# Performance work log

Measured on AMD Instinct MI355X. Metric: run time of the kernel, lower is better.

The kernel has to match this reference:

```python
import jax, jax.numpy as jnp
import numpy as np
from jax.scipy.special import logsumexp

K, V, D, R = 512, 50257, 768, 192
S_ITERS = 10
LAMBDA_MAHAL = 0.3
GAMMA_SINKHORN = 0.3


def setup_inputs() -> dict:
    key = jax.random.key(0)
    ks = jax.random.split(key, 6)
    word_embeds = jax.random.normal(ks[0], (V, D), dtype=jnp.float32)
    # warm-start anchors: mean word embed + small noise (as in torch init)
    anchors = jnp.broadcast_to(word_embeds.mean(axis=0, keepdims=True), (K, D)) \
        + jax.random.normal(ks[1], (K, D), dtype=jnp.float32) * 0.05
    return {
        "word_embeds": word_embeds,
        "concept_anchors": anchors,
        "M_U": jax.random.normal(ks[2], (D, R), dtype=jnp.float32) * 0.01,
        "log_eps": jnp.float32(-1.5),
        "log_scale": jnp.float32(0.0),
        "topic_bias": jnp.zeros((K, 1), dtype=jnp.float32),
        "word_proj_w": jnp.eye(D, dtype=jnp.float32),
    }


def _normalize(x, eps=1e-12):
    n = jnp.sqrt(jnp.sum(x * x, axis=-1, keepdims=True))
    return x / jnp.maximum(n, eps)


def _mahalanobis_cost(A, B, M_U):
    # M = I + U U^T  (low-rank update); C[k,v] = (a-b)^T M (a-b)
    M = jnp.eye(A.shape[-1], dtype=A.dtype) + M_U @ M_U.T
    MA = A @ M          # [K, D]
    MB = B @ M          # [V, D]
    AA = jnp.sum(MA * A, axis=-1, keepdims=True)       # [K, 1]
    BB = jnp.sum(MB * B, axis=-1, keepdims=True).T     # [1, V]
    AB = MA @ B.T                                      # [K, V]
    return jax.nn.relu(AA + BB - 2.0 * AB)


def _sinkhorn_log(log_K):
    def body(_, carry):
        log_u, log_v = carry
        log_u = -logsumexp(log_K + log_v, axis=1, keepdims=True)  # [K,1]
        log_v = -logsumexp(log_K + log_u, axis=0, keepdims=True)  # [1,V]
        return log_u, log_v
    log_u0 = jnp.zeros((log_K.shape[0], 1), log_K.dtype)
    log_v0 = jnp.zeros((1, log_K.shape[1]), log_K.dtype)
    log_u, log_v = jax.lax.fori_loop(0, S_ITERS, body, (log_u0, log_v0))
    return log_K + log_u + log_v


def reference(word_embeds, concept_anchors, M_U, log_eps, log_scale,
              topic_bias, word_proj_w):
    w = _normalize(word_embeds @ word_proj_w.T)     # [V, D]
    a = _normalize(concept_anchors)                 # [K, D]
    scale = jnp.minimum(jnp.exp(log_scale), 20.0)
    direct_logits = scale * (a @ w.T) + topic_bias  # [K, V]
    mahal = _mahalanobis_cost(a, w, M_U)            # [K, V]
    eps = jax.nn.softplus(log_eps) + 0.001
    log_P = _sinkhorn_log(-mahal / eps)             # [K, V]
    logits = direct_logits - LAMBDA_MAHAL * mahal + GAMMA_SINKHORN * log_P
    logits = jnp.clip(logits, -30.0, 30.0)
    return jax.nn.softmax(logits, axis=-1)
```

## Files before the change

kernel.cpp:

```cpp
#include <hip/hip_runtime.h>
#include <math.h>

#define KK 512
#define VV 50257
#define VP 50272
#define DD 768
#define RR 192

#define LAM 0.3f
#define GAM 0.3f
#define L2E 1.44269504088896340736f
#define ENC_NEG_INF 0x007FFFFFu

typedef __bf16 bf16x8 __attribute__((ext_vector_type(8)));
typedef _Float16 f16x8 __attribute__((ext_vector_type(8)));
typedef _Float16 f16x2 __attribute__((ext_vector_type(2)));
typedef unsigned short u16x8 __attribute__((ext_vector_type(8)));
typedef float f32x4 __attribute__((ext_vector_type(4)));

static __device__ __forceinline__ float get_eps(const float* p_log_eps) {
  return log1pf(expf(p_log_eps[0])) + 0.001f;
}

static __device__ __forceinline__ float fast_exp2(float x) {
  return __builtin_amdgcn_exp2f(x);
}

static __device__ __forceinline__ unsigned enc_f(float f) {
  unsigned u = __builtin_bit_cast(unsigned, f);
  return (u & 0x80000000u) ? ~u : (u | 0x80000000u);
}
static __device__ __forceinline__ float dec_f(unsigned e) {
  unsigned u = (e & 0x80000000u) ? (e ^ 0x80000000u) : ~e;
  return __builtin_bit_cast(float, u);
}

static __device__ __forceinline__ unsigned short f2bf(float x) {
  unsigned u = __builtin_bit_cast(unsigned, x);
  u += 0x7fffu + ((u >> 16) & 1u);
  return (unsigned short)(u >> 16);
}
static __device__ __forceinline__ float bf2f(unsigned short h) {
  unsigned u = ((unsigned)h) << 16;
  return __builtin_bit_cast(float, u);
}

static __device__ __forceinline__ void gload_lds16(const void* g, void* l) {
  __builtin_amdgcn_global_load_lds(
      (const __attribute__((address_space(1))) unsigned int*)g,
      (__attribute__((address_space(3))) unsigned int*)l, 16, 0, 0);
}

__global__ __launch_bounds__(256)
void prep(const float* __restrict__ U, float* __restrict__ lv2,
          unsigned* __restrict__ slots, const float* __restrict__ anchors,
          _Float16* __restrict__ Ut16, _Float16* __restrict__ a16) {
  int bid = blockIdx.x;
  int t = threadIdx.x;
  if (bid < 576) {
    int idx = bid * 256 + t;
    int r = idx / DD;
    int d = idx - r * DD;
    Ut16[idx] = (_Float16)U[(size_t)d * RR + r];
  } else if (bid < 773) {
    int i = (bid - 576) * 256 + t;
    if (i < 50264) lv2[i] = 0.f;
  } else if (bid == 773) {
    if (t < 24) slots[t] = (t == 0) ? 0x80000000u : ENC_NEG_INF;
    if (t == 24) slots[24] = 1u;
  } else {
    int r = bid - 774;
    const float* x = anchors + (size_t)r * DD;
    float v0 = x[t], v1 = x[t + 256], v2 = x[t + 512];
    __shared__ float red[256];
    red[t] = v0 * v0 + v1 * v1 + v2 * v2;
    __syncthreads();
    for (int off = 128; off > 0; off >>= 1) {
      if (t < off) red[t] += red[t + off];
      __syncthreads();
    }
    float inv = 1.0f / fmaxf(sqrtf(red[0]), 1e-12f);
    _Float16* y = a16 + (size_t)r * DD;
    y[t] = (_Float16)(v0 * inv);
    y[t + 256] = (_Float16)(v1 * inv);
    y[t + 512] = (_Float16)(v2 * inv);
  }
}

__global__ __launch_bounds__(256)
void check_eye(const float* __restrict__ Wp, unsigned* __restrict__ flag) {
  int i = blockIdx.x * 256 + threadIdx.x;
  if (i >= DD * DD) return;
  int r = i / DD;
  int c = i - r * DD;
  float expect = (r == c) ? 1.f : 0.f;
  if (Wp[i] != expect) atomicAnd(flag, 0u);
}

#define BM 128
#define BN 128
#define BK 32
#define LDKB 40
#define LDK 40

__global__ __launch_bounds__(256, 2)
void gemm_we_fallback(const float* __restrict__ A, const float* __restrict__ B,
                      _Float16* __restrict__ C, int M, int N, int Kd,
                      const unsigned* __restrict__ eyeflag) {
  if (*eyeflag) return;
  __shared__ unsigned short As[2][BM][LDKB];
  __shared__ unsigned short Bs[2][BN][LDKB];
  const int tid = threadIdx.x;
  const int bm = blockIdx.y * BM;
  const int bn = blockIdx.x * BN;
  const int srow = tid >> 1;
  const int skb = (tid & 1) << 4;
  const int wave = tid >> 6;
  const int lane = tid & 63;
// ... 144 lines not shown
    *(f16x8*)&As[srow][skb] = a0; *(f16x8*)&As[srow][skb + 8] = a1;
    *(f16x8*)&Bs[srow][skb] = b0; *(f16x8*)&Bs[srow][skb + 8] = b1;
    __syncthreads();
    f16x8 Af[4], Bf[4];
#pragma unroll
    for (int i = 0; i < 4; ++i) {
      Af[i] = *(const f16x8*)&As[wm + i * 16 + lm][quad * 8];
      Bf[i] = *(const f16x8*)&Bs[wn + i * 16 + lm][quad * 8];
    }
#pragma unroll
    for (int i = 0; i < 4; ++i)
#pragma unroll
      for (int j = 0; j < 4; ++j)
        acc[i][j] = __builtin_amdgcn_mfma_f32_16x16x32_f16(Af[i], Bf[j], acc[i][j], 0, 0, 0);
  }
#pragma unroll
  for (int i = 0; i < 4; ++i)
#pragma unroll
    for (int j = 0; j < 4; ++j) {
      int col = bn + wn + j * 16 + lm;
#pragma unroll
      for (int r = 0; r < 4; ++r) {
        int row = bm + wm + i * 16 + quad * 4 + r;
        if (row < M && col < N) {
          if (F16OUT)
            ((_Float16*)Cv)[(size_t)row * N + col] = (_Float16)acc[i][j][r];
          else
            ((float*)Cv)[(size_t)row * N + col] = acc[i][j][r];
        }
      }
    }
}

__global__ __launch_bounds__(256, 2)
void gemm_sp(const _Float16* __restrict__ Aw, const _Float16* __restrict__ Bw,
             const _Float16* __restrict__ Au, const _Float16* __restrict__ Bu,
             float* __restrict__ Sd, _Float16* __restrict__ mhq,
             const float* __restrict__ AAv, const float* __restrict__ BBv,
             const float* __restrict__ tbias,
             const float* __restrict__ p_log_scale,
             const float* __restrict__ p_log_eps, int M, int N) {
  __shared__ _Float16 As[2][BM][32];
  __shared__ _Float16 Bs[2][BM][32];
  const int tid = threadIdx.x;
  const int bm = blockIdx.x * BM;
  const int bn = blockIdx.y * BN;
  const int wave = tid >> 6;
  const int lane = tid & 63;
  const int wm = (wave >> 1) << 6;
  const int wn = (wave & 1) << 6;
  const int lm = lane & 15;
  const int quad = lane >> 4;

  const int c0 = wave * 2;
  const int r0 = c0 * 16 + (lane >> 2);
  const int r1 = r0 + 16;
  const int gp = lane & 3;
  const int gg0 = gp ^ ((r0 >> 1) & 3);
  const int gg1 = gp ^ ((r1 >> 1) & 3);

  const _Float16* pAu0 = Au + (size_t)(bm + r0) * RR + gg0 * 8;
  const _Float16* pAu1 = Au + (size_t)(bm + r1) * RR + gg1 * 8;
  const _Float16* pBu0 = Bu + (size_t)(bn + r0) * RR + gg0 * 8;
  const _Float16* pBu1 = Bu + (size_t)(bn + r1) * RR + gg1 * 8;
  const _Float16* pAw0 = Aw + (size_t)(bm + r0) * DD + gg0 * 8;
  const _Float16* pAw1 = Aw + (size_t)(bm + r1) * DD + gg1 * 8;
  const _Float16* pBw0 = Bw + (size_t)(bn + r0) * DD + gg0 * 8;
  const _Float16* pBw1 = Bw + (size_t)(bn + r1) * DD + gg1 * 8;

  auto stage = [&](int t, int buf) {
// ... 52 lines not shown
      stage(t + 1, cur ^ 1);
      asm volatile("s_waitcnt vmcnt(4)" ::: "memory");
    } else {
      asm volatile("s_waitcnt vmcnt(0)" ::: "memory");
    }
    __builtin_amdgcn_s_barrier();
    asm volatile("" ::: "memory");
    f16x8 Af[4], Bf[4];
#pragma unroll
    for (int i = 0; i < 4; ++i) {
      int ra_ = wm + i * 16 + lm;
      int rb_ = wn + i * 16 + lm;
      Af[i] = *(const f16x8*)&As[cur][ra_][(quad ^ ((ra_ >> 1) & 3)) * 8];
      Bf[i] = *(const f16x8*)&Bs[cur][rb_][(quad ^ ((rb_ >> 1) & 3)) * 8];
    }
#pragma unroll
    for (int i = 0; i < 4; ++i)
#pragma unroll
      for (int j = 0; j < 4; ++j)
        accS[i][j] = __builtin_amdgcn_mfma_f32_16x16x32_f16(Af[i], Bf[j], accS[i][j], 0, 0, 0);
    asm volatile("" ::: "memory");
    __builtin_amdgcn_s_barrier();
  }

  float scale = fminf(expf(p_log_scale[0]), 20.f);
  float qs = L2E / get_eps(p_log_eps);
#pragma unroll
  for (int i = 0; i < 4; ++i)
#pragma unroll
    for (int j = 0; j < 4; ++j) {
      int col = bn + wn + j * 16 + lm;
      if (col >= N) continue;
      float BB = BBv[col];
#pragma unroll
      for (int r = 0; r < 4; ++r) {
        int row = bm + wm + i * 16 + quad * 4 + r;
        float S = accS[i][j][r];
        float mh = fmaxf(AAv[row] + BB - 2.f * (S + accP[i][j][r]), 0.f);
        Sd[(size_t)row * N + col] = fmaf(scale, S, tbias[row]);
        mhq[(size_t)row * VP + col] = (_Float16)(mh * qs);
      }
    }
}

__global__ __launch_bounds__(256, 2)
void gemm16_p(const _Float16* __restrict__ A, const _Float16* __restrict__ B,
              float* __restrict__ Sd, _Float16* __restrict__ mhq,
              const float* __restrict__ AAv, const float* __restrict__ BBv,
              const float* __restrict__ tbias,
              const float* __restrict__ p_log_scale,
              const float* __restrict__ p_log_eps, int M, int N, int Kd) {
  __shared__ _Float16 As[BM][LDK];
  __shared__ _Float16 Bs[BN][LDK];
  const int tid = threadIdx.x;
  const int bm = blockIdx.y * BM;
  const int bn = blockIdx.x * BN;
  const int srow = tid >> 1;
  const int skb = (tid & 1) << 4;
  const int wave = tid >> 6;
  const int lane = tid & 63;
  const int wm = (wave >> 1) << 6;
  const int wn = (wave & 1) << 6;
  const int lm = lane & 15;
  const int quad = lane >> 4;
  f32x4 acc[4][4];
#pragma unroll
  for (int i = 0; i < 4; ++i)
#pragma unroll
    for (int j = 0; j < 4; ++j) acc[i][j] = (f32x4){0.f, 0.f, 0.f, 0.f};
  const int ra = bm + srow;
  const int rb = bn + srow;
  for (int k0 = 0; k0 < Kd; k0 += BK) {
    f16x8 a0 = (f16x8)(_Float16)0, a1 = a0, b0 = a0, b1 = a0;
    if (ra < M) {
// ... 26 lines not shown
  for (int i = 0; i < 4; ++i)
#pragma unroll
    for (int j = 0; j < 4; ++j) {
      int col = bn + wn + j * 16 + lm;
      if (col >= N) continue;
      float BB = BBv[col];
#pragma unroll
      for (int r = 0; r < 4; ++r) {
        int row = bm + wm + i * 16 + quad * 4 + r;
        size_t idx = (size_t)row * N + col;
        float S = Sd[idx];
        float mh = fmaxf(AAv[row] + BB - 2.f * (S + acc[i][j][r]), 0.f);
        Sd[idx] = fmaf(scale, S, tbias[row]);
        mhq[(size_t)row * VP + col] = (_Float16)(mh * qs);
      }
    }
}

__global__ __launch_bounds__(256)
void row_sumsq16(const _Float16* __restrict__ X, float* __restrict__ out, int cols) {
  int r = blockIdx.x;
  int t = threadIdx.x;
  float x = (t < cols) ? (float)X[(size_t)r * cols + t] : 0.f;
  __shared__ float red[256];
  red[t] = x * x;
  __syncthreads();
  for (int off = 128; off > 0; off >>= 1) {
    if (t < off) red[t] += red[t + off];
    __syncthreads();
  }
  if (t == 0) out[r] = 1.0f + red[0];
}

__global__ __launch_bounds__(1024)
void sink_row(const _Float16* __restrict__ mhq, const float* __restrict__ lv2,
              float* __restrict__ lu2,
              const unsigned* __restrict__ Mv_slot, unsigned* __restrict__ Mu_slot) {
  int k = blockIdx.x;
  int t = threadIdx.x;
  float Mv2 = dec_f(*Mv_slot);
  const _Float16* row = mhq + (size_t)k * VP;
  float s[8] = {0.f, 0.f, 0.f, 0.f, 0.f, 0.f, 0.f, 0.f};
#pragma unroll
  for (int j = 0; j < 6; ++j) {
    int v = j * 8192 + t * 8;
    f16x8 hv = *(const f16x8*)(row + v);
    float4 l0 = *(const float4*)(lv2 + v);
    float4 l1 = *(const float4*)(lv2 + v + 4);
    float lv[8] = {l0.x, l0.y, l0.z, l0.w, l1.x, l1.y, l1.z, l1.w};
#pragma unroll
    for (int i = 0; i < 8; ++i)
      s[i] += fast_exp2(lv[i] - Mv2 - (float)hv[i]);
  }
  {
    int v = 49152 + t;
    s[0] += fast_exp2(lv2[v] - Mv2 - (float)row[v]);
    v = 50176 + t;
    if (v < VV) s[1] += fast_exp2(lv2[v] - Mv2 - (float)row[v]);
  }
  float sum = ((s[0] + s[1]) + (s[2] + s[3])) + ((s[4] + s[5]) + (s[6] + s[7]));
  __shared__ float red[1024];
  red[t] = sum;
  __syncthreads();
  for (int off = 512; off > 0; off >>= 1) {
    if (t < off) red[t] += red[t + off];
    __syncthreads();
  }
  if (t == 0) {
    float lu = -(Mv2 + log2f(red[0]));
    lu2[k] = lu;
    atomicMax(Mu_slot, enc_f(lu));
  }
}

__global__ __launch_bounds__(256)
void sink_col(const _Float16* __restrict__ mhq, const float* __restrict__ lu2,
              float* __restrict__ lv2,
              const unsigned* __restrict__ Mu_slot, unsigned* __restrict__ Mv_next) {
  __shared__ float lu_s[KK];
  int t = threadIdx.x;
  for (int i = t; i < KK; i += 256) lu_s[i] = lu2[i];
  __syncthreads();
  float Mu2 = dec_f(*Mu_slot);
  int cp = blockIdx.x * 64 + (t & 63);
  int v0 = cp * 2;
  int kc = t >> 6;
  float sA = 0.f, sB = 0.f;
  if (v0 < VV) {
    const _Float16* base = mhq + v0;
#pragma unroll 4
    for (int k = kc * 128; k < kc * 128 + 128; ++k) {
      f16x2 hv = *(const f16x2*)(base + (size_t)k * VP);
      float lu = lu_s[k] - Mu2;
      sA += fast_exp2(lu - (float)hv[0]);
      sB += fast_exp2(lu - (float)hv[1]);
    }
  }
  __shared__ float pA[256], pB[256];
  __shared__ unsigned em[64];
  pA[t] = sA; pB[t] = sB;
  __syncthreads();
  if (t < 64) {
    unsigned e = ENC_NEG_INF;
    if (v0 < VV) {
      float a = (pA[t] + pA[t + 64]) + (pA[t + 128] + pA[t + 192]);
      float lv = -(Mu2 + log2f(a));
      lv2[v0] = lv;
      e = enc_f(lv);
      if (v0 + 1 < VV) {
        float b = (pB[t] + pB[t + 64]) + (pB[t + 128] + pB[t + 192]);
        float lv1 = -(Mu2 + log2f(b));
        lv2[v0 + 1] = lv1;
        unsigned e1 = enc_f(lv1);
        if (e1 > e) e = e1;
      }
    }
    em[t] = e;
  }
  __syncthreads();
  for (int off = 32; off > 0; off >>= 1) {
    if (t < off && em[t + off] > em[t]) em[t] = em[t + off];
    __syncthreads();
  }
  if (t == 0) atomicMax(Mv_next, em[0]);
}

__global__ __launch_bounds__(1024)
void final_sum(const float* __restrict__ direct, const _Float16* __restrict__ mhq,
               const float* __restrict__ lu2, const float* __restrict__ lv2,
               float* __restrict__ row_s, const float* __restrict__ p_log_eps) {
  int k = blockIdx.x;
  int t = threadIdx.x;
  float eps = get_eps(p_log_eps);
  float c2 = (LAM * eps + GAM) / L2E;
  float c3 = GAM / L2E;
  float base_lu = c3 * lu2[k];
  const float* drow = direct + (size_t)k * VV;
  const _Float16* mrow = mhq + (size_t)k * VP;
  float s[8] = {0.f, 0.f, 0.f, 0.f, 0.f, 0.f, 0.f, 0.f};
#pragma unroll
  for (int j = 0; j < 6; ++j) {
    int v = j * 8192 + t * 8;
    f16x8 hv = *(const f16x8*)(mrow + v);
    float4 d0 = *(const float4*)(drow + v);
    float4 d1 = *(const float4*)(drow + v + 4);
    float4 l0 = *(const float4*)(lv2 + v);
    float4 l1 = *(const float4*)(lv2 + v + 4);
    float dd[8] = {d0.x, d0.y, d0.z, d0.w, d1.x, d1.y, d1.z, d1.w};
    float lv[8] = {l0.x, l0.y, l0.z, l0.w, l1.x, l1.y, l1.z, l1.w};
#pragma unroll
    for (int i = 0; i < 8; ++i) {
      float x = fmaf(-c2, (float)hv[i], fmaf(c3, lv[i], dd[i] + base_lu));
      x = fminf(30.f, fmaxf(-30.f, x));
      s[i] += fast_exp2(fmaf(x, L2E, -30.f * L2E));
    }
  }
  {
    int v = 49152 + t;
    float x = fmaf(-c2, (float)mrow[v], fmaf(c3, lv2[v], drow[v] + base_lu));
    x = fminf(30.f, fmaxf(-30.f, x));
    s[0] += fast_exp2(fmaf(x, L2E, -30.f * L2E));
    v = 50176 + t;
    if (v < VV) {
      x = fmaf(-c2, (float)mrow[v], fmaf(c3, lv2[v], drow[v] + base_lu));
      x = fminf(30.f, fmaxf(-30.f, x));
      s[1] += fast_exp2(fmaf(x, L2E, -30.f * L2E));
    }
  }
  float sum = ((s[0] + s[1]) + (s[2] + s[3])) + ((s[4] + s[5]) + (s[6] + s[7]));
  __shared__ float red[1024];
  red[t] = sum;
  __syncthreads();
  for (int off = 512; off > 0; off >>= 1) {
    if (t < off) red[t] += red[t + off];
    __syncthreads();
  }
  if (t == 0) row_s[k] = red[0];
}

__global__ __launch_bounds__(256)
void final_write(float* __restrict__ out, const _Float16* __restrict__ mhq,
                 const float* __restrict__ lu2, const float* __restrict__ lv2,
                 const float* __restrict__ row_s, const float* __restrict__ p_log_eps) {
  int v = blockIdx.x * 256 + threadIdx.x;
  int k = blockIdx.y;
  if (v >= VV) return;
  float eps = get_eps(p_log_eps);
  float c2 = (LAM * eps + GAM) / L2E;
  float c3 = GAM / L2E;
  size_t idx = (size_t)k * VV + v;
  float x = fmaf(-c2, (float)mhq[(size_t)k * VP + v],
                 fmaf(c3, lv2[v], out[idx] + c3 * lu2[k]));
  x = fminf(30.f, fmaxf(-30.f, x));
  out[idx] = fast_exp2(fmaf(x, L2E, -30.f * L2E)) / row_s[k];
}

extern "C" void kernel_launch(void* const* d_in, const int* in_sizes, int n_in,
                              void* d_out, int out_size, void* d_ws, size_t ws_size,
                              hipStream_t stream) {
  (void)in_sizes; (void)n_in; (void)out_size;
  const float* WE        = (const float*)d_in[0];
  const float* anchors   = (const float*)d_in[1];
  const float* MU        = (const float*)d_in[2];
  const float* log_eps   = (const float*)d_in[3];
  const float* log_scale = (const float*)d_in[4];
  const float* tbias     = (const float*)d_in[5];
  const float* Wp        = (const float*)d_in[6];
  float* out = (float*)d_out;

  const size_t H_W16 = (size_t)VV * DD;
  const size_t H_MHQ = (size_t)KK * VP;
  const size_t H_WU  = (size_t)VV * RR;
  const size_t H_A16 = (size_t)KK * DD;
  const size_t H_AU  = (size_t)KK * RR;
  const size_t H_UT  = (size_t)RR * DD;
  const size_t FB_FLOATS = 102064 + 32;
  const size_t need_roomy =
      2 * (H_W16 + H_MHQ + H_WU + H_A16 + H_AU + H_UT) + 4 * FB_FLOATS;
  const bool roomy = ws_size >= need_roomy;

  _Float16* hb = (_Float16*)d_ws;
  _Float16* w16 = hb;
  size_t ho = H_W16;
  _Float16* mhq;
  if (roomy) { mhq = hb + ho; ho += H_MHQ; }
  else       { mhq = hb; }
  _Float16* wU16 = hb + ho; ho += H_WU;
  _Float16* a16  = hb + ho; ho += H_A16;
  _Float16* aU16 = hb + ho; ho += H_AU;
  _Float16* Ut16 = hb + ho; ho += H_UT;
  float* fb = (float*)(hb + ho);
  float* BBv   = fb;
  float* AAv   = fb + 50264;
  float* lu2   = fb + 50776;
  float* lv2   = fb + 51288;
  float* row_s = fb + 101552;
  unsigned* slots = (unsigned*)(fb + 102064);
  unsigned* Mv_slots = slots;
  unsigned* Mu_slots = slots + 12;
  unsigned* eye_flag = slots + 24;

  const int VB = (VV + 255) / 256;
  const int MB_V = (VV + BM - 1) / BM;

  prep<<<1286, 256, 0, stream>>>(MU, lv2, slots, anchors, Ut16, a16);
  check_eye<<<(DD * DD + 255) / 256, 256, 0, stream>>>(Wp, eye_flag);
  gemm_we_fallback<<<dim3(DD / BN, MB_V), 256, 0, stream>>>(WE, Wp, w16, VV, DD, DD, eye_flag);
  norm_w<<<VV, 256, 0, stream>>>(WE, w16, eye_flag);
  gemm16<1><<<dim3(2, MB_V), 256, 0, stream>>>(w16, Ut16, wU16, VV, RR, DD);
  gemm16<1><<<dim3(2, 4), 256, 0, stream>>>(a16, Ut16, aU16, KK, RR, DD);
  row_sumsq16<<<VV, 256, 0, stream>>>(wU16, BBv, RR);
  row_sumsq16<<<KK, 256, 0, stream>>>(aU16, AAv, RR);
  if (roomy) {
    gemm_sp<<<dim3(4, MB_V), 256, 0, stream>>>(a16, w16, aU16, wU16, out, mhq,
                                               AAv, BBv, tbias, log_scale,
                                               log_eps, KK, VV);
  } else {
    gemm16<0><<<dim3(MB_V, 4), 256, 0, stream>>>(a16, w16, out, KK, VV, DD);
    gemm16_p<<<dim3(MB_V, 4), 256, 0, stream>>>(aU16, wU16, out, mhq, AAv, BBv,
                                                tbias, log_scale, log_eps, KK, VV, RR);
  }
  for (int it = 0; it < 10; ++it) {
    sink_row<<<KK, 1024, 0, stream>>>(mhq, lv2, lu2, Mv_slots + it, Mu_slots + it);
    sink_col<<<MB_V, 256, 0, stream>>>(mhq, lu2, lv2, Mu_slots + it, Mv_slots + it + 1);
  }
  final_sum<<<KK, 1024, 0, stream>>>(out, mhq, lu2, lv2, row_s, log_eps);
  final_write<<<dim3(VB, KK), 256, 0, stream>>>(out, mhq, lu2, lv2, row_s, log_eps);
}
```

Before: 910.3 us.

## Fuse Sinkhorn iterations and final softmax into one persistent grid-barrier kernel

```diff
diff --git a/kernel.cpp b/kernel.cpp
--- a/kernel.cpp
+++ b/kernel.cpp
@@ -12,6 +12,9 @@
 #define L2E 1.44269504088896340736f
 #define ENC_NEG_INF 0x007FFFFFu
 
+#define SBLK 256
+#define CPB 197
+
 typedef __bf16 bf16x8 __attribute__((ext_vector_type(8)));
 typedef _Float16 f16x8 __attribute__((ext_vector_type(8)));
 typedef _Float16 f16x2 __attribute__((ext_vector_type(2)));
@@ -51,10 +54,27 @@
       (__attribute__((address_space(3))) unsigned int*)l, 16, 0, 0);
 }
 
+static __device__ __forceinline__ void gbar(unsigned* cnt, unsigned* gen) {
+  __syncthreads();
+  if (threadIdx.x == 0) {
+    unsigned g = __hip_atomic_load(gen, __ATOMIC_RELAXED, __HIP_MEMORY_SCOPE_AGENT);
+    unsigned a = __hip_atomic_fetch_add(cnt, 1u, __ATOMIC_ACQ_REL, __HIP_MEMORY_SCOPE_AGENT);
+    if (a == SBLK - 1) {
+      __hip_atomic_store(cnt, 0u, __ATOMIC_RELAXED, __HIP_MEMORY_SCOPE_AGENT);
+      __hip_atomic_fetch_add(gen, 1u, __ATOMIC_ACQ_REL, __HIP_MEMORY_SCOPE_AGENT);
+    } else {
+      while (__hip_atomic_load(gen, __ATOMIC_ACQUIRE, __HIP_MEMORY_SCOPE_AGENT) == g)
+        __builtin_amdgcn_s_sleep(2);
+    }
+  }
+  __syncthreads();
+}
+
 __global__ __launch_bounds__(256)
 void prep(const float* __restrict__ U, float* __restrict__ lv2,
           unsigned* __restrict__ slots, const float* __restrict__ anchors,
-          _Float16* __restrict__ Ut16, _Float16* __restrict__ a16) {
+          _Float16* __restrict__ Ut16, _Float16* __restrict__ a16,
+          float* __restrict__ SS) {
   int bid = blockIdx.x;
   int t = threadIdx.x;
   if (bid < 576) {
@@ -68,7 +88,8 @@
   } else if (bid == 773) {
     if (t < 24) slots[t] = (t == 0) ? 0x80000000u : ENC_NEG_INF;
     if (t == 24) slots[24] = 1u;
-  } else {
+    if (t >= 25 && t < 32) slots[t] = 0u;
+  } else if (bid < 1286) {
     int r = bid - 774;
     const float* x = anchors + (size_t)r * DD;
     float v0 = x[t], v1 = x[t + 256], v2 = x[t + 512];
@@ -84,6 +105,9 @@
     y[t] = (_Float16)(v0 * inv);
     y[t + 256] = (_Float16)(v1 * inv);
     y[t + 512] = (_Float16)(v2 * inv);
+  } else {
+    int idx = (bid - 1286) * 256 + t;
+    if (idx < 11 * KK) SS[idx] = 0.f;
   }
 }
 
@@ -516,167 +540,134 @@
   if (t == 0) out[r] = 1.0f + red[0];
 }
 
-__global__ __launch_bounds__(1024)
-void sink_row(const _Float16* __restrict__ mhq, const float* __restrict__ lv2,
-              float* __restrict__ lu2,
-              const unsigned* __restrict__ Mv_slot, unsigned* __restrict__ Mu_slot) {
-  int k = blockIdx.x;
-  int t = threadIdx.x;
-  float Mv2 = dec_f(*Mv_slot);
-  const _Float16* row = mhq + (size_t)k * VP;
-  float s[8] = {0.f, 0.f, 0.f, 0.f, 0.f, 0.f, 0.f, 0.f};
-#pragma unroll
-  for (int j = 0; j < 6; ++j) {
-    int v = j * 8192 + t * 8;
-    f16x8 hv = *(const f16x8*)(row + v);
-    float4 l0 = *(const float4*)(lv2 + v);
-    float4 l1 = *(const float4*)(lv2 + v + 4);
-    float lv[8] = {l0.x, l0.y, l0.z, l0.w, l1.x, l1.y, l1.z, l1.w};
-#pragma unroll
-    for (int i = 0; i < 8; ++i)
-      s[i] += fast_exp2(lv[i] - Mv2 - (float)hv[i]);
-  }
-  {
-    int v = 49152 + t;
-    s[0] += fast_exp2(lv2[v] - Mv2 - (float)row[v]);
-    v = 50176 + t;
-    if (v < VV) s[1] += fast_exp2(lv2[v] - Mv2 - (float)row[v]);
-  }
-  float sum = ((s[0] + s[1]) + (s[2] + s[3])) + ((s[4] + s[5]) + (s[6] + s[7]));
+__global__ __launch_bounds__(1024, 4)
+void sink_fused(const _Float16* __restrict__ mhq, float* __restrict__ out,
+                float* __restrict__ SS, unsigned* __restrict__ slots,
+                const float* __restrict__ p_log_eps) {
+  const int t = threadIdx.x;
+  const int wave = t >> 6;
+  const int lane = t & 63;
+  const int v0 = blockIdx.x * CPB;
+  const int k0 = wave * 32;
+  unsigned* Mv_slots = slots;
+  unsigned* bar_cnt = slots + 25;
+  unsigned* bar_gen = slots + 26;
+
+  __shared__ float lus[KK];
+  __shared__ float part[16][CPB];
   __shared__ float red[1024];
-  red[t] = sum;
-  __syncthreads();
-  for (int off = 512; off > 0; off >>= 1) {
-    if (t < off) red[t] += red[t + off];
-    __syncthreads();
-  }
-  if (t == 0) {
-    float lu = -(Mv2 + log2f(red[0]));
-    lu2[k] = lu;
-    atomicMax(Mu_slot, enc_f(lu));
-  }
-}
-
-__global__ __launch_bounds__(256)
-void sink_col(const _Float16* __restrict__ mhq, const float* __restrict__ lu2,
-              float* __restrict__ lv2,
-              const unsigned* __restrict__ Mu_slot, unsigned* __restrict__ Mv_next) {
-  __shared__ float lu_s[KK];
-  int t = threadIdx.x;
-  for (int i = t; i < KK; i += 256) lu_s[i] = lu2[i];
-  __syncthreads();
-  float Mu2 = dec_f(*Mu_slot);
-  int cp = blockIdx.x * 64 + (t & 63);
-  int v0 = cp * 2;
-  int kc = t >> 6;
-  float sA = 0.f, sB = 0.f;
-  if (v0 < VV) {
-    const _Float16* base = mhq + v0;
-#pragma unroll 4
-    for (int k = kc * 128; k < kc * 128 + 128; ++k) {
-      f16x2 hv = *(const f16x2*)(base + (size_t)k * VP);
-      float lu = lu_s[k] - Mu2;
-      sA += fast_exp2(lu - (float)hv[0]);
-      sB += fast_exp2(lu - (float)hv[1]);
-    }
-  }
-  __shared__ float pA[256], pB[256];
-  __shared__ unsigned em[64];
-  pA[t] = sA; pB[t] = sB;
-  __syncthreads();
-  if (t < 64) {
-    unsigned e = ENC_NEG_INF;
-    if (v0 < VV) {
-      float a = (pA[t] + pA[t + 64]) + (pA[t + 128] + pA[t + 192]);
-      float lv = -(Mu2 + log2f(a));
-      lv2[v0] = lv;
-      e = enc_f(lv);
-      if (v0 + 1 < VV) {
-        float b = (pB[t] + pB[t + 64]) + (pB[t + 128] + pB[t + 192]);
-        float lv1 = -(Mu2 + log2f(b));
-        lv2[v0 + 1] = lv1;
-        unsigned e1 = enc_f(lv1);
-        if (e1 > e) e = e1;
+
+  int cs[4]; float lv_reg[4]; bool cval[4];
+#pragma unroll
+  for (int j = 0; j < 4; ++j) {
+    int cl = lane + 64 * j;
+    bool v = (cl < CPB) && (v0 + cl < VV);
+    cval[j] = v;
+    cs[j] = v ? (v0 + cl) : v0;
+    lv_reg[j] = 0.f;
+  }
+
+  for (int it = 0; it < 10; ++it) {
+    float Mv2 = dec_f(__hip_atomic_load(Mv_slots + it, __ATOMIC_ACQUIRE,
+                                        __HIP_MEMORY_SCOPE_AGENT));
+    float lvm[4];
+#pragma unroll
+    for (int j = 0; j < 4; ++j) lvm[j] = cval[j] ? (lv_reg[j] - Mv2) : -1e30f;
+    for (int r = k0; r < k0 + 32; ++r) {
+      const _Float16* mr = mhq + (size_t)r * VP;
+      float s = 0.f;
+#pragma unroll
+      for (int j = 0; j < 4; ++j)
+        s += fast_exp2(lvm[j] - (float)mr[cs[j]]);
+#pragma unroll
+      for (int off = 32; off > 0; off >>= 1) s += __shfl_xor(s, off);
+      if (lane == 0) atomicAdd(&SS[it * KK + r], s);
+    }
+    gbar(bar_cnt, bar_gen);
+    if (t < KK)
+      lus[t] = -(Mv2 + log2f(__hip_atomic_load(&SS[it * KK + t],
+                                               __ATOMIC_RELAXED,
+                                               __HIP_MEMORY_SCOPE_AGENT)));
+    __syncthreads();
+    if (t < 512) red[t] = lus[t];
+    __syncthreads();
+    for (int off = 256; off > 0; off >>= 1) {
+      if (t < off) red[t] = fmaxf(red[t], red[t + off]);
+      __syncthreads();
+    }
+    float Mu2 = red[0];
+    __syncthreads();
+    float ps[4] = {0.f, 0.f, 0.f, 0.f};
+    for (int k = k0; k < k0 + 32; ++k) {
+      float lm = lus[k] - Mu2;
+      const _Float16* mr = mhq + (size_t)k * VP;
+#pragma unroll
+      for (int j = 0; j < 4; ++j)
+        ps[j] += fast_exp2(lm - (float)mr[cs[j]]);
+    }
+#pragma unroll
+    for (int j = 0; j < 4; ++j) {
+      int cl = lane + 64 * j;
+      if (cl < CPB) part[wave][cl] = ps[j];
+    }
+    __syncthreads();
+    float mymax = -1e38f;
+#pragma unroll
+    for (int j = 0; j < 4; ++j) {
+      if (cval[j]) {
+        float ssum = 0.f;
+#pragma unroll
+        for (int w = 0; w < 16; ++w) ssum += part[w][lane + 64 * j];
+        float lv = -(Mu2 + log2f(ssum));
+        lv_reg[j] = lv;
+        mymax = fmaxf(mymax, lv);
       }
     }
-    em[t] = e;
-  }
-  __syncthreads();
-  for (int off = 32; off > 0; off >>= 1) {
-    if (t < off && em[t + off] > em[t]) em[t] = em[t + off];
-    __syncthreads();
-  }
-  if (t == 0) atomicMax(Mv_next, em[0]);
-}
-
-__global__ __launch_bounds__(1024)
-void final_sum(const float* __restrict__ direct, const _Float16* __restrict__ mhq,
-               const float* __restrict__ lu2, const float* __restrict__ lv2,
-               float* __restrict__ row_s, const float* __restrict__ p_log_eps) {
-  int k = blockIdx.x;
-  int t = threadIdx.x;
+    if (wave == 0 && it < 9) {
+#pragma unroll
+      for (int off = 32; off > 0; off >>= 1)
+        mymax = fmaxf(mymax, __shfl_xor(mymax, off));
+      if (lane == 0) atomicMax(Mv_slots + it + 1, enc_f(mymax));
+    }
+    gbar(bar_cnt, bar_gen);
+  }
   float eps = get_eps(p_log_eps);
   float c2 = (LAM * eps + GAM) / L2E;
   float c3 = GAM / L2E;
-  float base_lu = c3 * lu2[k];
-  const float* drow = direct + (size_t)k * VV;
-  const _Float16* mrow = mhq + (size_t)k * VP;
-  float s[8] = {0.f, 0.f, 0.f, 0.f, 0.f, 0.f, 0.f, 0.f};
-#pragma unroll
-  for (int j = 0; j < 6; ++j) {
-    int v = j * 8192 + t * 8;
-    f16x8 hv = *(const f16x8*)(mrow + v);
-    float4 d0 = *(const float4*)(drow + v);
-    float4 d1 = *(const float4*)(drow + v + 4);
-    float4 l0 = *(const float4*)(lv2 + v);
-    float4 l1 = *(const float4*)(lv2 + v + 4);
-    float dd[8] = {d0.x, d0.y, d0.z, d0.w, d1.x, d1.y, d1.z, d1.w};
-    float lv[8] = {l0.x, l0.y, l0.z, l0.w, l1.x, l1.y, l1.z, l1.w};
-#pragma unroll
-    for (int i = 0; i < 8; ++i) {
-      float x = fmaf(-c2, (float)hv[i], fmaf(c3, lv[i], dd[i] + base_lu));
+  for (int r = k0; r < k0 + 32; ++r) {
+    const float* drow = out + (size_t)r * VV;
+    const _Float16* mr = mhq + (size_t)r * VP;
+    float base = c3 * lus[r];
+    float s = 0.f;
+#pragma unroll
+    for (int j = 0; j < 4; ++j) {
+      float x = fmaf(-c2, (float)mr[cs[j]], fmaf(c3, lv_reg[j], drow[cs[j]] + base));
       x = fminf(30.f, fmaxf(-30.f, x));
-      s[i] += fast_exp2(fmaf(x, L2E, -30.f * L2E));
-    }
-  }
-  {
-    int v = 49152 + t;
-    float x = fmaf(-c2, (float)mrow[v], fmaf(c3, lv2[v], drow[v] + base_lu));
-    x = fminf(30.f, fmaxf(-30.f, x));
-    s[0] += fast_exp2(fmaf(x, L2E, -30.f * L2E));
-    v = 50176 + t;
-    if (v < VV) {
-      x = fmaf(-c2, (float)mrow[v], fmaf(c3, lv2[v], drow[v] + base_lu));
+      float term = fast_exp2(fmaf(x, L2E, -30.f * L2E));
+      s += cval[j] ? term : 0.f;
+    }
+#pragma unroll
+    for (int off = 32; off > 0; off >>= 1) s += __shfl_xor(s, off);
+    if (lane == 0) atomicAdd(&SS[10 * KK + r], s);
+  }
+  gbar(bar_cnt, bar_gen);
+  if (t < KK)
+    red[t] = __hip_atomic_load(&SS[10 * KK + t], __ATOMIC_RELAXED,
+                               __HIP_MEMORY_SCOPE_AGENT);
+  __syncthreads();
+  for (int k = k0; k < k0 + 32; ++k) {
+    float* orow = out + (size_t)k * VV;
+    const _Float16* mr = mhq + (size_t)k * VP;
+    float base = c3 * lus[k];
+    float rs = red[k];
+#pragma unroll
+    for (int j = 0; j < 4; ++j) {
+      if (!cval[j]) continue;
+      float x = fmaf(-c2, (float)mr[cs[j]], fmaf(c3, lv_reg[j], orow[cs[j]] + base));
       x = fminf(30.f, fmaxf(-30.f, x));
-      s[1] += fast_exp2(fmaf(x, L2E, -30.f * L2E));
-    }
-  }
-  float sum = ((s[0] + s[1]) + (s[2] + s[3])) + ((s[4] + s[5]) + (s[6] + s[7]));
-  __shared__ float red[1024];
-  red[t] = sum;
-  __syncthreads();
-  for (int off = 512; off > 0; off >>= 1) {
-    if (t < off) red[t] += red[t + off];
-    __syncthreads();
-  }
-  if (t == 0) row_s[k] = red[0];
-}
-
-__global__ __launch_bounds__(256)
-void final_write(float* __restrict__ out, const _Float16* __restrict__ mhq,
-                 const float* __restrict__ lu2, const float* __restrict__ lv2,
-                 const float* __restrict__ row_s, const float* __restrict__ p_log_eps) {
-  int v = blockIdx.x * 256 + threadIdx.x;
-  int k = blockIdx.y;
-  if (v >= VV) return;
-  float eps = get_eps(p_log_eps);
-  float c2 = (LAM * eps + GAM) / L2E;
-  float c3 = GAM / L2E;
-  size_t idx = (size_t)k * VV + v;
-  float x = fmaf(-c2, (float)mhq[(size_t)k * VP + v],
-                 fmaf(c3, lv2[v], out[idx] + c3 * lu2[k]));
-  x = fminf(30.f, fmaxf(-30.f, x));
-  out[idx] = fast_exp2(fmaf(x, L2E, -30.f * L2E)) / row_s[k];
+      orow[cs[j]] = fast_exp2(fmaf(x, L2E, -30.f * L2E)) / rs;
+    }
+  }
 }
 
 extern "C" void kernel_launch(void* const* d_in, const int* in_sizes, int n_in,
@@ -698,7 +689,7 @@
   const size_t H_A16 = (size_t)KK * DD;
   const size_t H_AU  = (size_t)KK * RR;
   const size_t H_UT  = (size_t)RR * DD;
-  const size_t FB_FLOATS = 102064 + 32;
+  const size_t FB_FLOATS = 102064 + 32 + 11 * KK;
   const size_t need_roomy =
       2 * (H_W16 + H_MHQ + H_WU + H_A16 + H_AU + H_UT) + 4 * FB_FLOATS;
   const bool roomy = ws_size >= need_roomy;
@@ -716,18 +707,14 @@
   float* fb = (float*)(hb + ho);
   float* BBv   = fb;
   float* AAv   = fb + 50264;
-  float* lu2   = fb + 50776;
   float* lv2   = fb + 51288;
-  float* row_s = fb + 101552;
   unsigned* slots = (unsigned*)(fb + 102064);
-  unsigned* Mv_slots = slots;
-  unsigned* Mu_slots = slots + 12;
+  float* SS = fb + 102096;
   unsigned* eye_flag = slots + 24;
 
-  const int VB = (VV + 255) / 256;
   const int MB_V = (VV + BM - 1) / BM;
 
-  prep<<<1286, 256, 0, stream>>>(MU, lv2, slots, anchors, Ut16, a16);
+  prep<<<1308, 256, 0, stream>>>(MU, lv2, slots, anchors, Ut16, a16, SS);
   check_eye<<<(DD * DD + 255) / 256, 256, 0, stream>>>(Wp, eye_flag);
   gemm_we_fallback<<<dim3(DD / BN, MB_V), 256, 0, stream>>>(WE, Wp, w16, VV, DD, DD, eye_flag);
   norm_w<<<VV, 256, 0, stream>>>(WE, w16, eye_flag);
@@ -744,10 +731,5 @@
     gemm16_p<<<dim3(MB_V, 4), 256, 0, stream>>>(aU16, wU16, out, mhq, AAv, BBv,
                                                 tbias, log_scale, log_eps, KK, VV, RR);
   }
-  for (int it = 0; it < 10; ++it) {
-    sink_row<<<KK, 1024, 0, stream>>>(mhq, lv2, lu2, Mv_slots + it, Mu_slots + it);
-    sink_col<<<MB_V, 256, 0, stream>>>(mhq, lu2, lv2, Mu_slots + it, Mv_slots + it + 1);
-  }
-  final_sum<<<KK, 1024, 0, stream>>>(out, mhq, lu2, lv2, row_s, log_eps);
-  final_write<<<dim3(VB, KK), 256, 0, stream>>>(out, mhq, lu2, lv2, row_s, log_eps);
-}
+  sink_fused<<<SBLK, 1024, 0, stream>>>(mhq, out, SS, slots, log_eps);
+}
```

Result: slower. 2.752 ms (+202.3%).

## Write transposed fp16 cost matrix and use it for Sinkhorn column updates

Applied to the files above, without the earlier changes.

```diff
diff --git a/kernel.cpp b/kernel.cpp
--- a/kernel.cpp
+++ b/kernel.cpp
@@ -14,6 +14,7 @@
 
 typedef __bf16 bf16x8 __attribute__((ext_vector_type(8)));
 typedef _Float16 f16x8 __attribute__((ext_vector_type(8)));
+typedef _Float16 f16x4 __attribute__((ext_vector_type(4)));
 typedef _Float16 f16x2 __attribute__((ext_vector_type(2)));
 typedef unsigned short u16x8 __attribute__((ext_vector_type(8)));
 typedef float f32x4 __attribute__((ext_vector_type(4)));
@@ -294,10 +295,12 @@
     }
 }
 
+template <int WT>
 __global__ __launch_bounds__(256, 2)
 void gemm_sp(const _Float16* __restrict__ Aw, const _Float16* __restrict__ Bw,
              const _Float16* __restrict__ Au, const _Float16* __restrict__ Bu,
              float* __restrict__ Sd, _Float16* __restrict__ mhq,
+             _Float16* __restrict__ mhqT,
              const float* __restrict__ AAv, const float* __restrict__ BBv,
              const float* __restrict__ tbias,
              const float* __restrict__ p_log_scale,
@@ -416,14 +419,19 @@
       int col = bn + wn + j * 16 + lm;
       if (col >= N) continue;
       float BB = BBv[col];
+      f16x4 tq;
 #pragma unroll
       for (int r = 0; r < 4; ++r) {
         int row = bm + wm + i * 16 + quad * 4 + r;
         float S = accS[i][j][r];
         float mh = fmaxf(AAv[row] + BB - 2.f * (S + accP[i][j][r]), 0.f);
         Sd[(size_t)row * N + col] = fmaf(scale, S, tbias[row]);
-        mhq[(size_t)row * VP + col] = (_Float16)(mh * qs);
+        _Float16 q = (_Float16)(mh * qs);
+        mhq[(size_t)row * VP + col] = q;
+        tq[r] = q;
       }
+      if (WT)
+        *(f16x4*)(mhqT + (size_t)col * KK + (bm + wm + i * 16 + quad * 4)) = tq;
     }
 }
 
@@ -557,6 +565,41 @@
   }
 }
 
+__global__ __launch_bounds__(1024)
+void sink_colT(const _Float16* __restrict__ mhqT, const float* __restrict__ lu2,
+               float* __restrict__ lv2,
+               const unsigned* __restrict__ Mu_slot, unsigned* __restrict__ Mv_next) {
+  __shared__ float lum[KK];
+  __shared__ float wmax[16];
+  int t = threadIdx.x;
+  float Mu2 = dec_f(*Mu_slot);
+  if (t < KK) lum[t] = lu2[t] - Mu2;
+  __syncthreads();
+  int wave = t >> 6;
+  int lane = t & 63;
+  int v = blockIdx.x * 16 + wave;
+  float lv = -1e38f;
+  if (v < VV) {
+    f16x8 hv = *(const f16x8*)(mhqT + (size_t)v * KK + lane * 8);
+    const float* lp = &lum[lane * 8];
+    float s = 0.f;
+#pragma unroll
+    for (int j = 0; j < 8; ++j) s += fast_exp2(lp[j] - (float)hv[j]);
+#pragma unroll
+    for (int off = 32; off > 0; off >>= 1) s += __shfl_xor(s, off);
+    lv = -(Mu2 + log2f(s));
+    if (lane == 0) lv2[v] = lv;
+  }
+  if (lane == 0) wmax[wave] = lv;
+  __syncthreads();
+  if (t == 0) {
+    float m = wmax[0];
+#pragma unroll
+    for (int w = 1; w < 16; ++w) m = fmaxf(m, wmax[w]);
+    atomicMax(Mv_next, enc_f(m));
+  }
+}
+
 __global__ __launch_bounds__(256)
 void sink_col(const _Float16* __restrict__ mhq, const float* __restrict__ lu2,
               float* __restrict__ lv2,
@@ -694,6 +737,7 @@
 
   const size_t H_W16 = (size_t)VV * DD;
   const size_t H_MHQ = (size_t)KK * VP;
+  const size_t H_MHT = (size_t)VV * KK;
   const size_t H_WU  = (size_t)VV * RR;
   const size_t H_A16 = (size_t)KK * DD;
   const size_t H_AU  = (size_t)KK * RR;
@@ -701,6 +745,8 @@
   const size_t FB_FLOATS = 102064 + 32;
   const size_t need_roomy =
       2 * (H_W16 + H_MHQ + H_WU + H_A16 + H_AU + H_UT) + 4 * FB_FLOATS;
+  const size_t need_roomy2 = need_roomy + 2 * H_MHT;
+  const bool roomy2 = ws_size >= need_roomy2;
   const bool roomy = ws_size >= need_roomy;
 
   _Float16* hb = (_Float16*)d_ws;
@@ -709,6 +755,8 @@
   _Float16* mhq;
   if (roomy) { mhq = hb + ho; ho += H_MHQ; }
   else       { mhq = hb; }
+  _Float16* mhqT = hb + ho;
+  if (roomy2) ho += H_MHT;
   _Float16* wU16 = hb + ho; ho += H_WU;
   _Float16* a16  = hb + ho; ho += H_A16;
   _Float16* aU16 = hb + ho; ho += H_AU;
@@ -726,6 +774,7 @@
 
   const int VB = (VV + 255) / 256;
   const int MB_V = (VV + BM - 1) / BM;
+  const int NBT = (VV + 15) / 16;
 
   prep<<<1286, 256, 0, stream>>>(MU, lv2, slots, anchors, Ut16, a16);
   check_eye<<<(DD * DD + 255) / 256, 256, 0, stream>>>(Wp, eye_flag);
@@ -735,18 +784,30 @@
   gemm16<1><<<dim3(2, 4), 256, 0, stream>>>(a16, Ut16, aU16, KK, RR, DD);
   row_sumsq16<<<VV, 256, 0, stream>>>(wU16, BBv, RR);
   row_sumsq16<<<KK, 256, 0, stream>>>(aU16, AAv, RR);
-  if (roomy) {
-    gemm_sp<<<dim3(4, MB_V), 256, 0, stream>>>(a16, w16, aU16, wU16, out, mhq,
-                                               AAv, BBv, tbias, log_scale,
-                                               log_eps, KK, VV);
+  if (roomy2) {
+    gemm_sp<1><<<dim3(4, MB_V), 256, 0, stream>>>(a16, w16, aU16, wU16, out, mhq,
+                                                  mhqT, AAv, BBv, tbias, log_scale,
+                                                  log_eps, KK, VV);
+    for (int it = 0; it < 10; ++it) {
+      sink_row<<<KK, 1024, 0, stream>>>(mhq, lv2, lu2, Mv_slots + it, Mu_slots + it);
+      sink_colT<<<NBT, 1024, 0, stream>>>(mhqT, lu2, lv2, Mu_slots + it, Mv_slots + it + 1);
+    }
+  } else if (roomy) {
+    gemm_sp<0><<<dim3(4, MB_V), 256, 0, stream>>>(a16, w16, aU16, wU16, out, mhq,
+                                                  mhqT, AAv, BBv, tbias, log_scale,
+                                                  log_eps, KK, VV);
+    for (int it = 0; it < 10; ++it) {
+      sink_row<<<KK, 1024, 0, stream>>>(mhq, lv2, lu2, Mv_slots + it, Mu_slots + it);
+      sink_col<<<MB_V, 256, 0, stream>>>(mhq, lu2, lv2, Mu_slots + it, Mv_slots + it + 1);
+    }
   } else {
     gemm16<0><<<dim3(MB_V, 4), 256, 0, stream>>>(a16, w16, out, KK, VV, DD);
     gemm16_p<<<dim3(MB_V, 4), 256, 0, stream>>>(aU16, wU16, out, mhq, AAv, BBv,
                                                 tbias, log_scale, log_eps, KK, VV, RR);
-  }
-  for (int it = 0; it < 10; ++it) {
-    sink_row<<<KK, 1024, 0, stream>>>(mhq, lv2, lu2, Mv_slots + it, Mu_slots + it);
-    sink_col<<<MB_V, 256, 0, stream>>>(mhq, lu2, lv2, Mu_slots + it, Mv_slots + it + 1);
+    for (int it = 0; it < 10; ++it) {
+      sink_row<<<KK, 1024, 0, stream>>>(mhq, lv2, lu2, Mv_slots + it, Mu_slots + it);
+      sink_col<<<MB_V, 256, 0, stream>>>(mhq, lu2, lv2, Mu_slots + it, Mv_slots + it + 1);
+    }
   }
   final_sum<<<KK, 1024, 0, stream>>>(out, mhq, lu2, lv2, row_s, log_eps);
   final_write<<<dim3(VB, KK), 256, 0, stream>>>(out, mhq, lu2, lv2, row_s, log_eps);
```

Measured after the change: 1.154 ms. 1.27x slower.

## Fuse Sinkhorn row and column passes into one tile-resident kernel per iteration

Applied to the files above, without the earlier changes.

```diff
diff --git a/kernel.cpp b/kernel.cpp
--- a/kernel.cpp
+++ b/kernel.cpp
@@ -10,11 +10,9 @@
 #define LAM 0.3f
 #define GAM 0.3f
 #define L2E 1.44269504088896340736f
-#define ENC_NEG_INF 0x007FFFFFu
 
 typedef __bf16 bf16x8 __attribute__((ext_vector_type(8)));
 typedef _Float16 f16x8 __attribute__((ext_vector_type(8)));
-typedef _Float16 f16x2 __attribute__((ext_vector_type(2)));
 typedef unsigned short u16x8 __attribute__((ext_vector_type(8)));
 typedef float f32x4 __attribute__((ext_vector_type(4)));
 
@@ -24,15 +22,6 @@
 
 static __device__ __forceinline__ float fast_exp2(float x) {
   return __builtin_amdgcn_exp2f(x);
-}
-
-static __device__ __forceinline__ unsigned enc_f(float f) {
-  unsigned u = __builtin_bit_cast(unsigned, f);
-  return (u & 0x80000000u) ? ~u : (u | 0x80000000u);
-}
-static __device__ __forceinline__ float dec_f(unsigned e) {
-  unsigned u = (e & 0x80000000u) ? (e ^ 0x80000000u) : ~e;
-  return __builtin_bit_cast(float, u);
 }
 
 static __device__ __forceinline__ unsigned short f2bf(float x) {
@@ -52,9 +41,10 @@
 }
 
 __global__ __launch_bounds__(256)
-void prep(const float* __restrict__ U, float* __restrict__ lv2,
-          unsigned* __restrict__ slots, const float* __restrict__ anchors,
-          _Float16* __restrict__ Ut16, _Float16* __restrict__ a16) {
+void prep(const float* __restrict__ U, unsigned* __restrict__ slots,
+          const float* __restrict__ anchors,
+          _Float16* __restrict__ Ut16, _Float16* __restrict__ a16,
+          float* __restrict__ Rbuf) {
   int bid = blockIdx.x;
   int t = threadIdx.x;
   if (bid < 576) {
@@ -62,14 +52,13 @@
     int r = idx / DD;
     int d = idx - r * DD;
     Ut16[idx] = (_Float16)U[(size_t)d * RR + r];
-  } else if (bid < 773) {
+  } else if (bid < 598) {
     int i = (bid - 576) * 256 + t;
-    if (i < 50264) lv2[i] = 0.f;
-  } else if (bid == 773) {
-    if (t < 24) slots[t] = (t == 0) ? 0x80000000u : ENC_NEG_INF;
-    if (t == 24) slots[24] = 1u;
+    if (i < 11 * KK) Rbuf[i] = 0.f;
+  } else if (bid == 598) {
+    if (t == 0) slots[24] = 1u;
   } else {
-    int r = bid - 774;
+    int r = bid - 599;
     const float* x = anchors + (size_t)r * DD;
     float v0 = x[t], v1 = x[t + 256], v2 = x[t + 512];
     __shared__ float red[256];
@@ -517,30 +506,23 @@
 }
 
 __global__ __launch_bounds__(1024)
-void sink_row(const _Float16* __restrict__ mhq, const float* __restrict__ lv2,
-              float* __restrict__ lu2,
-              const unsigned* __restrict__ Mv_slot, unsigned* __restrict__ Mu_slot) {
+void sink_row0(const _Float16* __restrict__ mhq, float* __restrict__ R0) {
   int k = blockIdx.x;
   int t = threadIdx.x;
-  float Mv2 = dec_f(*Mv_slot);
   const _Float16* row = mhq + (size_t)k * VP;
   float s[8] = {0.f, 0.f, 0.f, 0.f, 0.f, 0.f, 0.f, 0.f};
 #pragma unroll
   for (int j = 0; j < 6; ++j) {
     int v = j * 8192 + t * 8;
     f16x8 hv = *(const f16x8*)(row + v);
-    float4 l0 = *(const float4*)(lv2 + v);
-    float4 l1 = *(const float4*)(lv2 + v + 4);
-    float lv[8] = {l0.x, l0.y, l0.z, l0.w, l1.x, l1.y, l1.z, l1.w};
-#pragma unroll
-    for (int i = 0; i < 8; ++i)
-      s[i] += fast_exp2(lv[i] - Mv2 - (float)hv[i]);
+#pragma unroll
+    for (int i = 0; i < 8; ++i) s[i] += fast_exp2(-(float)hv[i]);
   }
   {
     int v = 49152 + t;
-    s[0] += fast_exp2(lv2[v] - Mv2 - (float)row[v]);
+    s[0] += fast_exp2(-(float)row[v]);
     v = 50176 + t;
-    if (v < VV) s[1] += fast_exp2(lv2[v] - Mv2 - (float)row[v]);
+    if (v < VV) s[1] += fast_exp2(-(float)row[v]);
   }
   float sum = ((s[0] + s[1]) + (s[2] + s[3])) + ((s[4] + s[5]) + (s[6] + s[7]));
   __shared__ float red[1024];
@@ -550,116 +532,123 @@
     if (t < off) red[t] += red[t + off];
     __syncthreads();
   }
-  if (t == 0) {
-    float lu = -(Mv2 + log2f(red[0]));
-    lu2[k] = lu;
-    atomicMax(Mu_slot, enc_f(lu));
-  }
-}
-
-__global__ __launch_bounds__(256)
-void sink_col(const _Float16* __restrict__ mhq, const float* __restrict__ lu2,
-              float* __restrict__ lv2,
-              const unsigned* __restrict__ Mu_slot, unsigned* __restrict__ Mv_next) {
+  if (t == 0) R0[k] = red[0];
+}
+
+template <int FINAL>
+__global__ __launch_bounds__(1024, 2)
+void sink_step(const _Float16* __restrict__ mhq, const float* __restrict__ Rprev,
+               float* __restrict__ Rout, float* __restrict__ lv2out,
+               float* __restrict__ lu2out, const float* __restrict__ direct,
+               const float* __restrict__ p_log_eps) {
+  __shared__ _Float16 qt[512][64];
   __shared__ float lu_s[KK];
-  int t = threadIdx.x;
-  for (int i = t; i < KK; i += 256) lu_s[i] = lu2[i];
+  __shared__ float partC[16][64];
+  __shared__ float lv_s[64];
+  const int t = threadIdx.x;
+  const int wave = t >> 6;
+  const int lane = t & 63;
+  const int c = lane & 7;
+  const int kr = (wave << 3) + (lane >> 3);
+  const int cbase = blockIdx.x * 64;
+  if (t < KK) lu_s[t] = -log2f(Rprev[t]);
   __syncthreads();
-  float Mu2 = dec_f(*Mu_slot);
-  int cp = blockIdx.x * 64 + (t & 63);
-  int v0 = cp * 2;
-  int kc = t >> 6;
-  float sA = 0.f, sB = 0.f;
-  if (v0 < VV) {
-    const _Float16* base = mhq + v0;
-#pragma unroll 4
-    for (int k = kc * 128; k < kc * 128 + 128; ++k) {
-      f16x2 hv = *(const f16x2*)(base + (size_t)k * VP);
-      float lu = lu_s[k] - Mu2;
-      sA += fast_exp2(lu - (float)hv[0]);
-      sB += fast_exp2(lu - (float)hv[1]);
-    }
-  }
-  __shared__ float pA[256], pB[256];
-  __shared__ unsigned em[64];
-  pA[t] = sA; pB[t] = sB;
+  const _Float16* gsrc = mhq + cbase + c * 8;
+  float acc[8] = {0.f, 0.f, 0.f, 0.f, 0.f, 0.f, 0.f, 0.f};
+#pragma unroll
+  for (int s = 0; s < 4; ++s) {
+    int k = kr + s * 128;
+    f16x8 hv = *(const f16x8*)(gsrc + (size_t)k * VP);
+    *(f16x8*)&qt[k][c * 8] = hv;
+    float lu = lu_s[k];
+#pragma unroll
+    for (int j = 0; j < 8; ++j) acc[j] += fast_exp2(lu - (float)hv[j]);
+  }
+#pragma unroll
+  for (int j = 0; j < 8; ++j) {
+    acc[j] += __shfl_xor(acc[j], 8);
+    acc[j] += __shfl_xor(acc[j], 16);
+    acc[j] += __shfl_xor(acc[j], 32);
+  }
+  if (lane < 8) {
+#pragma unroll
+    for (int j = 0; j < 8; ++j) partC[wave][lane * 8 + j] = acc[j];
+  }
   __syncthreads();
   if (t < 64) {
-    unsigned e = ENC_NEG_INF;
-    if (v0 < VV) {
-      float a = (pA[t] + pA[t + 64]) + (pA[t + 128] + pA[t + 192]);
-      float lv = -(Mu2 + log2f(a));
-      lv2[v0] = lv;
-      e = enc_f(lv);
-      if (v0 + 1 < VV) {
-        float b = (pB[t] + pB[t + 64]) + (pB[t + 128] + pB[t + 192]);
-        float lv1 = -(Mu2 + log2f(b));
-        lv2[v0 + 1] = lv1;
-        unsigned e1 = enc_f(lv1);
-        if (e1 > e) e = e1;
-      }
-    }
-    em[t] = e;
-  }
+    float s = 0.f;
+#pragma unroll
+    for (int w = 0; w < 16; ++w) s += partC[w][t];
+    float lv = (cbase + t < VV) ? -log2f(s) : -1e30f;
+    lv_s[t] = lv;
+    if (FINAL && cbase + t < VV) lv2out[cbase + t] = lv;
+  }
+  if (FINAL && blockIdx.x == 0 && t < KK) lu2out[t] = lu_s[t];
   __syncthreads();
-  for (int off = 32; off > 0; off >>= 1) {
-    if (t < off && em[t + off] > em[t]) em[t] = em[t + off];
-    __syncthreads();
-  }
-  if (t == 0) atomicMax(Mv_next, em[0]);
-}
-
-__global__ __launch_bounds__(1024)
-void final_sum(const float* __restrict__ direct, const _Float16* __restrict__ mhq,
-               const float* __restrict__ lu2, const float* __restrict__ lv2,
-               float* __restrict__ row_s, const float* __restrict__ p_log_eps) {
-  int k = blockIdx.x;
-  int t = threadIdx.x;
-  float eps = get_eps(p_log_eps);
-  float c2 = (LAM * eps + GAM) / L2E;
-  float c3 = GAM / L2E;
-  float base_lu = c3 * lu2[k];
-  const float* drow = direct + (size_t)k * VV;
-  const _Float16* mrow = mhq + (size_t)k * VP;
-  float s[8] = {0.f, 0.f, 0.f, 0.f, 0.f, 0.f, 0.f, 0.f};
-#pragma unroll
-  for (int j = 0; j < 6; ++j) {
-    int v = j * 8192 + t * 8;
-    f16x8 hv = *(const f16x8*)(mrow + v);
-    float4 d0 = *(const float4*)(drow + v);
-    float4 d1 = *(const float4*)(drow + v + 4);
-    float4 l0 = *(const float4*)(lv2 + v);
-    float4 l1 = *(const float4*)(lv2 + v + 4);
-    float dd[8] = {d0.x, d0.y, d0.z, d0.w, d1.x, d1.y, d1.z, d1.w};
-    float lv[8] = {l0.x, l0.y, l0.z, l0.w, l1.x, l1.y, l1.z, l1.w};
-#pragma unroll
-    for (int i = 0; i < 8; ++i) {
-      float x = fmaf(-c2, (float)hv[i], fmaf(c3, lv[i], dd[i] + base_lu));
-      x = fminf(30.f, fmaxf(-30.f, x));
-      s[i] += fast_exp2(fmaf(x, L2E, -30.f * L2E));
-    }
-  }
-  {
-    int v = 49152 + t;
-    float x = fmaf(-c2, (float)mrow[v], fmaf(c3, lv2[v], drow[v] + base_lu));
-    x = fminf(30.f, fmaxf(-30.f, x));
-    s[0] += fast_exp2(fmaf(x, L2E, -30.f * L2E));
-    v = 50176 + t;
-    if (v < VV) {
-      x = fmaf(-c2, (float)mrow[v], fmaf(c3, lv2[v], drow[v] + base_lu));
-      x = fminf(30.f, fmaxf(-30.f, x));
-      s[1] += fast_exp2(fmaf(x, L2E, -30.f * L2E));
-    }
-  }
-  float sum = ((s[0] + s[1]) + (s[2] + s[3])) + ((s[4] + s[5]) + (s[6] + s[7]));
-  __shared__ float red[1024];
-  red[t] = sum;
-  __syncthreads();
-  for (int off = 512; off > 0; off >>= 1) {
-    if (t < off) red[t] += red[t + off];
-    __syncthreads();
-  }
-  if (t == 0) row_s[k] = red[0];
+  float lvr[8];
+#pragma unroll
+  for (int j = 0; j < 8; ++j) lvr[j] = lv_s[c * 8 + j];
+  const bool edge = (cbase + 64 > VV);
+  if (!FINAL) {
+#pragma unroll
+    for (int s = 0; s < 4; ++s) {
+      int k = kr + s * 128;
+      f16x8 hv = *(const f16x8*)&qt[k][c * 8];
+      float sum = 0.f;
+      if (!edge) {
+#pragma unroll
+        for (int j = 0; j < 8; ++j) sum += fast_exp2(lvr[j] - (float)hv[j]);
+      } else {
+#pragma unroll
+        for (int j = 0; j < 8; ++j) {
+          float term = fast_exp2(lvr[j] - (float)hv[j]);
+          sum += (cbase + c * 8 + j < VV) ? term : 0.f;
+        }
+      }
+      sum += __shfl_xor(sum, 1);
+      sum += __shfl_xor(sum, 2);
+      sum += __shfl_xor(sum, 4);
+      if (c == 0) atomicAdd(&Rout[k], sum);
+    }
+  } else {
+    float eps = get_eps(p_log_eps);
+    float c2 = (LAM * eps + GAM) / L2E;
+    float c3 = GAM / L2E;
+#pragma unroll
+    for (int s = 0; s < 4; ++s) {
+      int k = kr + s * 128;
+      f16x8 hv = *(const f16x8*)&qt[k][c * 8];
+      float bl = c3 * lu_s[k];
+      const float* dp = direct + (size_t)k * VV + cbase + c * 8;
+      float sum = 0.f;
+      if (!edge) {
+        float d[8];
+        *(float4*)&d[0] = *(const float4*)dp;
+        *(float4*)&d[4] = *(const float4*)(dp + 4);
+#pragma unroll
+        for (int j = 0; j < 8; ++j) {
+          float x = fmaf(-c2, (float)hv[j], fmaf(c3, lvr[j], d[j] + bl));
+          x = fminf(30.f, fmaxf(-30.f, x));
+          sum += fast_exp2(fmaf(x, L2E, -30.f * L2E));
+        }
+      } else {
+#pragma unroll
+        for (int j = 0; j < 8; ++j) {
+          int col = cbase + c * 8 + j;
+          bool v = col < VV;
+          float d = v ? dp[j] : 0.f;
+          float x = fmaf(-c2, (float)hv[j], fmaf(c3, lvr[j], d + bl));
+          x = fminf(30.f, fmaxf(-30.f, x));
+          float term = fast_exp2(fmaf(x, L2E, -30.f * L2E));
+          sum += v ? term : 0.f;
+        }
+      }
+      sum += __shfl_xor(sum, 1);
+      sum += __shfl_xor(sum, 2);
+      sum += __shfl_xor(sum, 4);
+      if (c == 0) atomicAdd(&Rout[k], sum);
+    }
+  }
 }
 
 __global__ __launch_bounds__(256)
@@ -698,7 +687,7 @@
   const size_t H_A16 = (size_t)KK * DD;
   const size_t H_AU  = (size_t)KK * RR;
   const size_t H_UT  = (size_t)RR * DD;
-  const size_t FB_FLOATS = 102064 + 32;
+  const size_t FB_FLOATS = 102096 + 11 * KK + 64;
   const size_t need_roomy =
       2 * (H_W16 + H_MHQ + H_WU + H_A16 + H_AU + H_UT) + 4 * FB_FLOATS;
   const bool roomy = ws_size >= need_roomy;
@@ -718,16 +707,15 @@
   float* AAv   = fb + 50264;
   float* lu2   = fb + 50776;
   float* lv2   = fb + 51288;
-  float* row_s = fb + 101552;
   unsigned* slots = (unsigned*)(fb + 102064);
-  unsigned* Mv_slots = slots;
-  unsigned* Mu_slots = slots + 12;
+  float* Rbuf  = fb + 102096;
   unsigned* eye_flag = slots + 24;
 
   const int VB = (VV + 255) / 256;
   const int MB_V = (VV + BM - 1) / BM;
-
-  prep<<<1286, 256, 0, stream>>>(MU, lv2, slots, anchors, Ut16, a16);
+  const int NSB = (VV + 63) / 64;
+
+  prep<<<1111, 256, 0, stream>>>(MU, slots, anchors, Ut16, a16, Rbuf);
   check_eye<<<(DD * DD + 255) / 256, 256, 0, stream>>>(Wp, eye_flag);
   gemm_we_fallback<<<dim3(DD / BN, MB_V), 256, 0, stream>>>(WE, Wp, w16, VV, DD, DD, eye_flag);
   norm_w<<<VV, 256, 0, stream>>>(WE, w16, eye_flag);
@@ -744,10 +732,12 @@
     gemm16_p<<<dim3(MB_V, 4), 256, 0, stream>>>(aU16, wU16, out, mhq, AAv, BBv,
                                                 tbias, log_scale, log_eps, KK, VV, RR);
   }
-  for (int it = 0; it < 10; ++it) {
-    sink_row<<<KK, 1024, 0, stream>>>(mhq, lv2, lu2, Mv_slots + it, Mu_slots + it);
-    sink_col<<<MB_V, 256, 0, stream>>>(mhq, lu2, lv2, Mu_slots + it, Mv_slots + it + 1);
-  }
-  final_sum<<<KK, 1024, 0, stream>>>(out, mhq, lu2, lv2, row_s, log_eps);
-  final_write<<<dim3(VB, KK), 256, 0, stream>>>(out, mhq, lu2, lv2, row_s, log_eps);
-}
+  sink_row0<<<KK, 1024, 0, stream>>>(mhq, Rbuf);
+  for (int it = 1; it <= 9; ++it)
+    sink_step<0><<<NSB, 1024, 0, stream>>>(mhq, Rbuf + (it - 1) * KK,
+                                           Rbuf + it * KK, lv2, lu2, out, log_eps);
+  sink_step<1><<<NSB, 1024, 0, stream>>>(mhq, Rbuf + 9 * KK, Rbuf + 10 * KK,
+                                         lv2, lu2, out, log_eps);
+  final_write<<<dim3(VB, KK), 256, 0, stream>>>(out, mhq, lu2, lv2,
+                                                Rbuf + 10 * KK, log_eps);
+}
```

Result: slower. 1.031 ms (+13.2%).
